# Kernel tuning notes

Measured on AMD Instinct MI355X. Metric: run time of the kernel, lower is better.

The kernel has to match this reference:

```python
import jax, jax.numpy as jnp
import numpy as np

B, S, CIN, WIDTH, COUT = 8, 256, 3, 64, 1
MODES, BW = 32, 3


def _dct_matrix(n):
    # orthonormal DCT-II matrix; inverse = transpose (DCT-III)
    k = np.arange(n)[:, None].astype(np.float64)
    x = np.arange(n)[None, :].astype(np.float64)
    m = np.sqrt(2.0 / n) * np.cos(np.pi * (x + 0.5) * k / n)
    m[0] *= 1.0 / np.sqrt(2.0)
    return jnp.asarray(m, dtype=jnp.float32)

DCT = _dct_matrix(S)  # [S, S]


def T_fwd(u):  # u: [B, C, H, W] -> spectral coefficients
    u = jnp.einsum('kh,bchw->bckw', DCT, u)
    return jnp.einsum('lw,bckw->bckl', DCT, u)


def T_inv(c):  # inverse transform (orthonormal => transpose)
    c = jnp.einsum('kh,bckw->bchw', DCT, c)
    return jnp.einsum('lw,bclw->bclh', DCT, c).transpose(0, 1, 3, 2)


def T_inv2(c):
    # straightforward version: apply M^T along both spatial dims
    c = jnp.einsum('kh,bckl->bchl', DCT, c)
    return jnp.einsum('lw,bchl->bchw', DCT, c)


def gelu(x):
    return jax.nn.gelu(x, approximate=False)


def pseudo_spectra(u, w, cout):
    # u: [B, Cin, S, S]; w: [Cin*BW*BW, cout, MODES*MODES]
    b = T_fwd(u)
    p = MODES + BW - 1
    bp = b[:, :, :p, :p]  # pad_slices (triL=0)
    # im2col matching torch.nn.Unfold channel-major ordering (c, ki, kj)
    patches = jnp.stack([bp[:, :, i:i + MODES, j:j + MODES]
                         for i in range(BW) for j in range(BW)], axis=2)
    bs, cin = u.shape[0], u.shape[1]
    xp = patches.reshape(bs, cin * BW * BW, MODES * MODES)
    om = jnp.einsum('bix,iox->box', xp, w).reshape(bs, cout, MODES, MODES)
    out = jnp.zeros((bs, cout, S, S), u.dtype).at[:, :, :MODES, :MODES].set(om)
    return T_inv2(out)


def conv1x1(x, w, b):
    return jnp.einsum('oi,bihw->bohw', w, x) + b[None, :, None, None]


def setup_inputs() -> dict:
    key = jax.random.key(0)
    ks = jax.random.split(key, 20)
    mm = MODES * MODES
    inp = {'x': jax.random.normal(ks[0], (B, S, S, CIN), dtype=jnp.float32)}
    # PseudoSpectra weights: scale * U[0,1), scale = 1/(in*out)
    inp['wl'] = jax.random.uniform(ks[1], (CIN * BW * BW, WIDTH - CIN, mm), dtype=jnp.float32) / (CIN * (WIDTH - CIN))
    for i in range(4):
        inp[f'wc{i}'] = jax.random.uniform(ks[2 + i], (WIDTH * BW * BW, WIDTH, mm), dtype=jnp.float32) / (WIDTH * WIDTH)
    for i in range(4):
        inp[f'pw{i}'] = jax.random.normal(ks[6 + i], (WIDTH, WIDTH), dtype=jnp.float32) * 0.05
        inp[f'pb{i}'] = jnp.zeros((WIDTH,), dtype=jnp.float32)
    inp['fc1_w'] = jax.random.normal(ks[10], (WIDTH, 128), dtype=jnp.float32) * 0.05
    inp['fc1_b'] = jnp.zeros((128,), dtype=jnp.float32)
    inp['fc2_w'] = jax.random.normal(ks[11], (128, COUT), dtype=jnp.float32) * 0.05
    inp['fc2_b'] = jnp.zeros((COUT,), dtype=jnp.float32)
    return inp


def reference(x, wl, wc0, wc1, wc2, wc3,
              pw0, pb0, pw1, pb1, pw2, pb2, pw3, pb3,
              fc1_w, fc1_b, fc2_w, fc2_b):
    h = x.transpose(0, 3, 1, 2)  # [B, CIN, S, S]
    h = jnp.concatenate([h, gelu(pseudo_spectra(h, wl, WIDTH - CIN))], axis=1)
    h = h + gelu(conv1x1(h, pw0, pb0) + pseudo_spectra(h, wc0, WIDTH))
    h = h + gelu(conv1x1(h, pw1, pb1) + pseudo_spectra(h, wc1, WIDTH))
    h = h + gelu(conv1x1(h, pw2, pb2) + pseudo_spectra(h, wc2, WIDTH))
    h = h + gelu(conv1x1(h, pw3, pb3) + pseudo_spectra(h, wc3, WIDTH))
    h = h.transpose(0, 2, 3, 1)  # [B, S, S, WIDTH]
    h = gelu(h @ fc1_w + fc1_b)
    h = h @ fc2_w + fc2_b  # [B, S, S, COUT]
    y = h.transpose(0, 3, 1, 2)
    y = T_fwd(T_inv2(y))  # T(T.inv(.)) along spatial dims, as in source
    return y.transpose(0, 2, 3, 1)
```

## Files before the change

kernel.cpp:

```cpp
#include <hip/hip_runtime.h>
#include <math.h>

#define BB 8
#define S 256
#define CIN 3
#define W64 64
#define MODES 32
#define PP 34
#define KPAD 36
#define KPB 40

typedef __attribute__((ext_vector_type(8))) short bfrag;
typedef __attribute__((ext_vector_type(16))) float f32x16;

__device__ __forceinline__ float gelu_f(float x){
    float z = fabsf(x) * 0.70710678118654752f;
    float t = 1.0f / (1.0f + 0.3275911f * z);
    float p = ((((1.061405429f * t - 1.453152027f) * t) + 1.421413741f) * t
               - 0.284496736f) * t + 0.254829592f;
    float e = __expf(-z * z);
    float erf = 1.0f - p * t * e;
    erf = copysignf(erf, x);
    return 0.5f * x * (1.0f + erf);
}

__device__ __forceinline__ void split_bf(float x, short &hi, short &lo){
    unsigned u = __float_as_uint(x);
    unsigned r = u + 0x7FFFu + ((u >> 16) & 1u);
    hi = (short)(r >> 16);
    float hf = __uint_as_float(r & 0xFFFF0000u);
    float l = x - hf;
    unsigned v = __float_as_uint(l);
    unsigned s2 = v + 0x7FFFu + ((v >> 16) & 1u);
    lo = (short)(s2 >> 16);
}

__device__ __forceinline__ void split8(float4 a, float4 b, bfrag &hv, bfrag &lv){
    short hi, lo;
    split_bf(a.x, hi, lo); hv[0] = hi; lv[0] = lo;
    split_bf(a.y, hi, lo); hv[1] = hi; lv[1] = lo;
    split_bf(a.z, hi, lo); hv[2] = hi; lv[2] = lo;
    split_bf(a.w, hi, lo); hv[3] = hi; lv[3] = lo;
    split_bf(b.x, hi, lo); hv[4] = hi; lv[4] = lo;
    split_bf(b.y, hi, lo); hv[5] = hi; lv[5] = lo;
    split_bf(b.z, hi, lo); hv[6] = hi; lv[6] = lo;
    split_bf(b.w, hi, lo); hv[7] = hi; lv[7] = lo;
}

__global__ void k_init_dt(float* __restrict__ dt, short* __restrict__ dth,
                          short* __restrict__ dtl){
    int tid = blockIdx.x * 256 + threadIdx.x;
    if (tid >= S * KPB) return;
    int h = tid / KPB, k = tid % KPB;
    double v = 0.0;
    if (k < PP) {
        v = sqrt(2.0 / (double)S) * cos(3.14159265358979323846 * (h + 0.5) * k / (double)S);
        if (k == 0) v *= 0.70710678118654752440;
    }
    float f = (float)v;
    if (k < KPAD) dt[h * KPAD + k] = f;
    short hi, lo; split_bf(f, hi, lo);
    dth[tid] = hi; dtl[tid] = lo;
}

__global__ void k_prep_pw(const float* __restrict__ pw, short* __restrict__ pwh,
                          short* __restrict__ pwl){
    int e = blockIdx.x * 256 + threadIdx.x;
    if (e >= 4096) return;
    short hi, lo; split_bf(pw[e], hi, lo);
    pwh[e] = hi; pwl[e] = lo;
}

__global__ void k_prep_fc1(const float* __restrict__ fc1w, short* __restrict__ f1h,
                           short* __restrict__ f1l){
    int e = blockIdx.x * 256 + threadIdx.x;
    if (e >= 8192) return;
    int i = e >> 7, j = e & 127;
    int n = j >> 5, ks = i >> 4;
    int l = (j & 31) + (((i & 15) >= 8) ? 32 : 0);
    int jr = i & 7;
    int idx = ((n * 4 + ks) * 64 + l) * 8 + jr;
    short hi, lo; split_bf(fc1w[e], hi, lo);
    f1h[idx] = hi; f1l[idx] = lo;
}

__global__ void k_copy_x(const float* __restrict__ x, float* __restrict__ h){
    int e = blockIdx.x * 256 + threadIdx.x;
    if (e >= BB * S * S * CIN) return;
    int px = e / CIN, c = e % CIN;
    h[(size_t)px * W64 + c] = x[e];
}

template<int C>
__global__ void k_fwd1(const float* __restrict__ src, float* __restrict__ tmp1,
                       const float* __restrict__ dt){
    int b = blockIdx.y;
    int idx = blockIdx.x * 256 + threadIdx.x;
    if (idx >= S * C) return;
    float acc[PP];
    #pragma unroll
    for (int k = 0; k < PP; k++) acc[k] = 0.f;
    const float* sp = src + (size_t)b * S * S * C + idx;
    for (int hh = 0; hh < S; hh++){
        float v = sp[(size_t)hh * S * C];
        const float* dr = dt + hh * KPAD;
        #pragma unroll
        for (int k = 0; k < PP; k++) acc[k] = fmaf(dr[k], v, acc[k]);
    }
    float* op = tmp1 + (size_t)b * PP * S * C + idx;
    #pragma unroll
    for (int k = 0; k < PP; k++) op[(size_t)k * S * C] = acc[k];
}

__global__ void k_fwd2_3(const float* __restrict__ tmp1, float* __restrict__ bp,
                         const float* __restrict__ dt){
    const int C = 3;
    int b = blockIdx.y;
    int idx = blockIdx.x * 256 + threadIdx.x;
    if (idx >= PP * C) return;
    int k = idx / C, c = idx % C;
    float acc[PP];
    #pragma unroll
    for (int l = 0; l < PP; l++) acc[l] = 0.f;
    const float* sp = tmp1 + ((size_t)b * PP + k) * S * C + c;
    for (int w = 0; w < S; w++){
        float v = sp[(size_t)w * C];
        const float* dr = dt + w * KPAD;
        #pragma unroll
        for (int l = 0; l < PP; l++) acc[l] = fmaf(dr[l], v, acc[l]);
    }
    float* op = bp + ((size_t)b * PP + k) * PP * C + c;
    #pragma unroll
    for (int l = 0; l < PP; l++) op[(size_t)l * C] = acc[l];
}

__global__ __launch_bounds__(256, 4) void k_fwd2_64(
        const float* __restrict__ tmp1, float* __restrict__ bp,
        const float* __restrict__ dt){
    const int C = 64;
    __shared__ float red[4 * PP * 66];
    int k = blockIdx.x, b = blockIdx.y;
    int t = threadIdx.x;
    int c = t & 63;
    int ws = __builtin_amdgcn_readfirstlane(t >> 6);
    float acc[PP];
    #pragma unroll
    for (int l = 0; l < PP; l++) acc[l] = 0.f;
    const float* sp = tmp1 + ((size_t)b * PP + k) * S * C + c;
    for (int w = ws * 64; w < ws * 64 + 64; w++){
        float v = sp[(size_t)w * C];
        const float* dr = dt + w * KPAD;
        #pragma unroll
        for (int l = 0; l < PP; l++) acc[l] = fmaf(dr[l], v, acc[l]);
    }
    #pragma unroll
    for (int l = 0; l < PP; l++) red[(ws * PP + l) * 66 + c] = acc[l];
    __syncthreads();
    float* op = bp + ((size_t)b * PP + k) * PP * C;
    for (int e = t; e < PP * C; e += 256){
        int l = e >> 6, cc = e & 63;
        op[e] = red[(0 * PP + l) * 66 + cc] + red[(1 * PP + l) * 66 + cc]
              + red[(2 * PP + l) * 66 + cc] + red[(3 * PP + l) * 66 + cc];
    }
}

template<int C, int CC>
__global__ void k_xp_gather(const float* __restrict__ bp, float* __restrict__ xp){
    __shared__ float lds[8 * 3 * PP * (CC + 1)];
    int k  = blockIdx.x;
    int c0 = blockIdx.y * CC;
    int t  = threadIdx.x;
    const int TOT = 8 * 3 * PP * CC;
    for (int e = t; e < TOT; e += 256){
        int b   = e / (3 * PP * CC);
        int r   = e % (3 * PP * CC);
        int row = r / (PP * CC);
        int r2  = r % (PP * CC);
        int l   = r2 / CC;
        int c   = r2 % CC;
        lds[((b * 3 + row) * PP + l) * (CC + 1) + c] =
            bp[(((size_t)b * PP + (k + row)) * PP + l) * C + c0 + c];
    }
    __syncthreads();
    int l = t >> 3;
    int b = t & 7;
    for (int c = 0; c < CC; c++){
        #pragma unroll
        for (int ij = 0; ij < 9; ij++){
            int i_ = ij / 3, j_ = ij % 3;
            int i  = (c0 + c) * 9 + ij;
            float v = lds[((b * 3 + i_) * PP + (l + j_)) * (CC + 1) + c];
            xp[((size_t)i * 1024 + k * 32 + l) * 8 + b] = v;
        }
    }
}

template<int ITOT, int O>
__global__ void k_om(const float* __restrict__ xp, const float* __restrict__ w,
                     float* __restrict__ part){
    int bx  = blockIdx.x;
    int klt = bx & 31;
    int ot  = (bx >> 5) & 7;
    int ns  = bx >> 8;
    const int ILEN = ITOT / 3;
    int t  = threadIdx.x;
    int kl = klt * 32 + (t & 31);
    int o  = ot * 8 + (t >> 5);
    if (o >= O) return;
    float a0=0,a1=0,a2=0,a3=0,a4=0,a5=0,a6=0,a7=0;
    const float* xpp = xp + ((size_t)(ns * ILEN) * 1024 + kl) * 8;
    const float* wp  = w + ((size_t)(ns * ILEN) * O + o) * 1024 + kl;
    #pragma unroll 4
    for (int i = 0; i < ILEN; i++){
        float4 xa = *(const float4*)(xpp + (size_t)i * 8192);
        float4 xb = *(const float4*)(xpp + (size_t)i * 8192 + 4);
        float wv  = wp[(size_t)i * O * 1024];
        a0 = fmaf(xa.x, wv, a0); a1 = fmaf(xa.y, wv, a1);
        a2 = fmaf(xa.z, wv, a2); a3 = fmaf(xa.w, wv, a3);
        a4 = fmaf(xb.x, wv, a4); a5 = fmaf(xb.y, wv, a5);
        a6 = fmaf(xb.z, wv, a6); a7 = fmaf(xb.w, wv, a7);
    }
    float* pp = part + (size_t)ns * 8 * 64 * 1024;
    pp[((size_t)0 * 64 + o) * 1024 + kl] = a0;
    pp[((size_t)1 * 64 + o) * 1024 + kl] = a1;
    pp[((size_t)2 * 64 + o) * 1024 + kl] = a2;
    pp[((size_t)3 * 64 + o) * 1024 + kl] = a3;
    pp[((size_t)4 * 64 + o) * 1024 + kl] = a4;
    pp[((size_t)5 * 64 + o) * 1024 + kl] = a5;
    pp[((size_t)6 * 64 + o) * 1024 + kl] = a6;
    pp[((size_t)7 * 64 + o) * 1024 + kl] = a7;
}

template<int O>
__global__ void k_inv1(const float* __restrict__ part, float* __restrict__ t2,
                       const float* __restrict__ dt){
    __shared__ float oms[32 * 65];
    const int N = 8 * 64 * 1024;
    int wc = blockIdx.x, k = blockIdx.y, b = blockIdx.z;
    int t = threadIdx.x;
    for (int e = t; e < 2048; e += 256){
        int o_ = e >> 5, l = e & 31;
        int idx = ((b * 64 + o_) << 10) + k * 32 + l;
        oms[l * 65 + o_] = part[idx] + part[N + idx] + part[2 * N + idx];
    }
    __syncthreads();
    int o  = t & 63;
    int wg = __builtin_amdgcn_readfirstlane(t >> 6);
    int wbase = wc * 32 + wg * 8;
    float acc[8];
    #pragma unroll
    for (int wj = 0; wj < 8; wj++) acc[wj] = 0.f;
    for (int l = 0; l < 32; l++){
        float ov = oms[l * 65 + o];
        #pragma unroll
        for (int wj = 0; wj < 8; wj++)
            acc[wj] = fmaf(dt[(wbase + wj) * KPAD + l], ov, acc[wj]);
    }
    if (o < O){
        #pragma unroll
        for (int wj = 0; wj < 8; wj++)
            t2[(((size_t)b * 32 + k) * S + wbase + wj) * 64 + o] = acc[wj];
    }
}

template<bool CONV>
__global__ __launch_bounds__(256, 5) void k_fused(
        const float* __restrict__ t2, float* __restrict__ h,
        const short* __restrict__ pwh, const short* __restrict__ pwl,
        const float* __restrict__ pb,
        const short* __restrict__ dth, const short* __restrict__ dtl){
    __shared__ short t2fh[8 * 64 * 8];
    __shared__ short t2fl[8 * 64 * 8];
    __shared__ short hsfh[CONV ? 8 * 64 * 8 : 1];
    __shared__ short hsfl[CONV ? 8 * 64 * 8 : 1];
    int wt = blockIdx.x, b = blockIdx.y;
    int t = threadIdx.x;

    #pragma unroll
    for (int e2 = 0; e2 < 2; e2++){
        int e = t + e2 * 256;
        int le = e & 63, ks = (e >> 6) & 1, ne = e >> 7;
        int oe = (ne & 1) * 32 + (le & 31);
        int we = wt * 2 + (ne >> 1);
        int k0 = ks * 16 + (le >> 5) * 8;
        bfrag hv, lv;
        #pragma unroll
        for (int j = 0; j < 8; j++){
            short hi, lo;
            split_bf(t2[((size_t)(b * 32 + k0 + j) * S + we) * 64 + oe], hi, lo);
            hv[j] = hi; lv[j] = lo;
        }
        int idx = ((ne * 2 + ks) * 64 + le) * 8;
        *(bfrag*)(t2fh + idx) = hv;
        *(bfrag*)(t2fl + idx) = lv;
    }

    int l = t & 63;
    int n = t >> 6;
    int oh = n & 1, wl = n >> 1;
    int o = oh * 32 + (l & 31);

    int ihalf = t & 7;
    int pxA = t >> 3;
    int pxB = pxA + 32;
    const float* hb = h + ((size_t)b * S * S + (size_t)wt * 2) * 64;
    size_t offA = ((size_t)(pxA >> 1) * S + (pxA & 1)) * 64 + ihalf * 8;
    size_t offB = ((size_t)(pxB >> 1) * S + (pxB & 1)) * 64 + ihalf * 8;
    float4 a0, a1, b0, b1;
    if (CONV){
        a0 = *(const float4*)(hb + offA);
        a1 = *(const float4*)(hb + offA + 4);
        b0 = *(const float4*)(hb + offB);
        b1 = *(const float4*)(hb + offB + 4);
    }

    for (int ht = 0; ht < 8; ht++){
        if (CONV){
            int ks = ihalf >> 1;
            int lh = (ihalf & 1) * 32;
            int g  = (pxA & 1) * 4 + ks;
            bfrag hv, lv;
            split8(a0, a1, hv, lv);
            int rowA = (pxA >> 1) + lh;
            *(bfrag*)(hsfh + (g * 64 + (rowA ^ g)) * 8) = hv;
            *(bfrag*)(hsfl + (g * 64 + (rowA ^ g)) * 8) = lv;
            split8(b0, b1, hv, lv);
            int rowB = (pxB >> 1) + lh;
            *(bfrag*)(hsfh + (g * 64 + (rowB ^ g)) * 8) = hv;
            *(bfrag*)(hsfl + (g * 64 + (rowB ^ g)) * 8) = lv;
        }
        __syncthreads();
        if (CONV && ht < 7){
            const float* hb2 = hb + (size_t)(ht + 1) * 32 * S * 64;
            a0 = *(const float4*)(hb2 + offA);
            a1 = *(const float4*)(hb2 + offA + 4);
            b0 = *(const float4*)(hb2 + offB);
            b1 = *(const float4*)(hb2 + offB + 4);
        }

        f32x16 acc = {0,0,0,0,0,0,0,0,0,0,0,0,0,0,0,0};

        int hh0 = ht * 32;
        #pragma unroll
        for (int ks = 0; ks < 2; ks++){
            int aoff = (hh0 + (l & 31)) * KPB + ks * 16 + (l >> 5) * 8;
            bfrag ah = *(const bfrag*)(dth + aoff);
            bfrag al = *(const bfrag*)(dtl + aoff);
            int boff = ((n * 2 + ks) * 64 + l) * 8;
            bfrag bh = *(const bfrag*)(t2fh + boff);
            bfrag bl = *(const bfrag*)(t2fl + boff);
            acc = __builtin_amdgcn_mfma_f32_32x32x16_bf16(ah, bh, acc, 0, 0, 0);
            acc = __builtin_amdgcn_mfma_f32_32x32x16_bf16(ah, bl, acc, 0, 0, 0);
            acc = __builtin_amdgcn_mfma_f32_32x32x16_bf16(al, bh, acc, 0, 0, 0);
        }

        if (CONV){
            #pragma unroll
            for (int ks = 0; ks < 4; ks++){
                int g = wl * 4 + ks;
                int aoff = (g * 64 + (l ^ g)) * 8;
                bfrag ah = *(const bfrag*)(hsfh + aoff);
                bfrag al = *(const bfrag*)(hsfl + aoff);
                int boff = o * 64 + ks * 16 + (l >> 5) * 8;
                bfrag bh = *(const bfrag*)(pwh + boff);
                bfrag bl = *(const bfrag*)(pwl + boff);
                acc = __builtin_amdgcn_mfma_f32_32x32x16_bf16(ah, bh, acc, 0, 0, 0);
                acc = __builtin_amdgcn_mfma_f32_32x32x16_bf16(ah, bl, acc, 0, 0, 0);
                acc = __builtin_amdgcn_mfma_f32_32x32x16_bf16(al, bh, acc, 0, 0, 0);
            }
            float pbv = pb[o];
            #pragma unroll
            for (int r = 0; r < 16; r++){
                int row = (r & 3) + 8 * (r >> 2) + 4 * (l >> 5);
                size_t pix = ((size_t)b * S + ht * 32 + row) * S + wt * 2 + wl;
                float res = h[pix * 64 + o];
                h[pix * 64 + o] = res + gelu_f(acc[r] + pbv);
            }
        } else {
            if (o < 61){
                #pragma unroll
                for (int r = 0; r < 16; r++){
                    int row = (r & 3) + 8 * (r >> 2) + 4 * (l >> 5);
                    size_t pix = ((size_t)b * S + ht * 32 + row) * S + wt * 2 + wl;
                    h[pix * 64 + 3 + o] = gelu_f(acc[r]);
                }
            }
        }
        __syncthreads();
    }
}

__global__ __launch_bounds__(256, 4) void k_mlp(
        const float* __restrict__ h, const short* __restrict__ f1h,
        const short* __restrict__ f1l, const float* __restrict__ fc1b,
        const float* __restrict__ fc2w, const float* __restrict__ fc2b,
        float* __restrict__ out){
    __shared__ short ah_[2 * 4 * 64 * 8];
    __shared__ short al_[2 * 4 * 64 * 8];
    __shared__ float red[2 * 64 * 33];
    size_t base = (size_t)blockIdx.x * 64;
    int t = threadIdx.x;
    const float* hrow = h + base * 64;
    #pragma unroll
    for (int e2 = 0; e2 < 2; e2++){
        int e = t + e2 * 256;
        int px = e >> 3, ih = e & 7;
        float4 v0 = *(const float4*)(hrow + px * 64 + ih * 8);
        float4 v1 = *(const float4*)(hrow + px * 64 + ih * 8 + 4);
        bfrag hv, lv;
        split8(v0, v1, hv, lv);
        int g = (px >> 5) * 4 + (ih >> 1);
        int row = (px & 31) + (ih & 1) * 32;
        *(bfrag*)(ah_ + (g * 64 + (row ^ g)) * 8) = hv;
        *(bfrag*)(al_ + (g * 64 + (row ^ g)) * 8) = lv;
    }
    __syncthreads();
    int l = t & 63;
    int w = t >> 6;
    int m = w >> 1;
    int n0 = (w & 1) * 2;
    f32x16 acc0 = {0,0,0,0,0,0,0,0,0,0,0,0,0,0,0,0};
    f32x16 acc1 = {0,0,0,0,0,0,0,0,0,0,0,0,0,0,0,0};
    #pragma unroll
    for (int ks = 0; ks < 4; ks++){
        int g = m * 4 + ks;
        int aoff = (g * 64 + (l ^ g)) * 8;
        bfrag ah = *(const bfrag*)(ah_ + aoff);
        bfrag al = *(const bfrag*)(al_ + aoff);
        int b0off = ((n0 * 4 + ks) * 64 + l) * 8;
        int b1off = (((n0 + 1) * 4 + ks) * 64 + l) * 8;
        bfrag b0h = *(const bfrag*)(f1h + b0off);
        bfrag b0l = *(const bfrag*)(f1l + b0off);
        bfrag b1h = *(const bfrag*)(f1h + b1off);
        bfrag b1l = *(const bfrag*)(f1l + b1off);
        acc0 = __builtin_amdgcn_mfma_f32_32x32x16_bf16(ah, b0h, acc0, 0, 0, 0);
        acc0 = __builtin_amdgcn_mfma_f32_32x32x16_bf16(ah, b0l, acc0, 0, 0, 0);
        acc0 = __builtin_amdgcn_mfma_f32_32x32x16_bf16(al, b0h, acc0, 0, 0, 0);
        acc1 = __builtin_amdgcn_mfma_f32_32x32x16_bf16(ah, b1h, acc1, 0, 0, 0);
        acc1 = __builtin_amdgcn_mfma_f32_32x32x16_bf16(ah, b1l, acc1, 0, 0, 0);
        acc1 = __builtin_amdgcn_mfma_f32_32x32x16_bf16(al, b1h, acc1, 0, 0, 0);
    }
    int j0 = n0 * 32 + (l & 31), j1 = j0 + 32;
    float b10 = fc1b[j0], b11 = fc1b[j1];
    float f20 = fc2w[j0], f21 = fc2w[j1];
    float* rb = red + (w & 1) * 64 * 33;
    #pragma unroll
    for (int r = 0; r < 16; r++){
        int row = (r & 3) + 8 * (r >> 2) + 4 * (l >> 5);
        rb[(m * 32 + row) * 33 + (l & 31)] =
            gelu_f(acc0[r] + b10) * f20 + gelu_f(acc1[r] + b11) * f21;
    }
    __syncthreads();
    if (t < 64){
        float s = fc2b[0];
        #pragma unroll
        for (int c = 0; c < 32; c++)
            s += red[t * 33 + c] + red[(64 + t) * 33 + c];
        out[base + t] = s;
    }
}

extern "C" void kernel_launch(void* const* d_in, const int* in_sizes, int n_in,
                              void* d_out, int out_size, void* d_ws, size_t ws_size,
                              hipStream_t stream) {
    const float* x    = (const float*)d_in[0];
    const float* wl   = (const float*)d_in[1];
    const float* wc[4] = {(const float*)d_in[2], (const float*)d_in[3],
                          (const float*)d_in[4], (const float*)d_in[5]};
    const float* pw[4] = {(const float*)d_in[6], (const float*)d_in[8],
                          (const float*)d_in[10], (const float*)d_in[12]};
    const float* pb[4] = {(const float*)d_in[7], (const float*)d_in[9],
                          (const float*)d_in[11], (const float*)d_in[13]};
    const float* fc1w = (const float*)d_in[14];
    const float* fc1b = (const float*)d_in[15];
    const float* fc2w = (const float*)d_in[16];
    const float* fc2b = (const float*)d_in[17];
    float* out = (float*)d_out;

    char* ws = (char*)d_ws;
    size_t off = 0;
    float* dt   = (float*)(ws + off); off += (size_t)S * KPAD * 4;
    short* dth  = (short*)(ws + off); off += (size_t)S * KPB * 2;
    short* dtl  = (short*)(ws + off); off += (size_t)S * KPB * 2;
    short* pwh  = (short*)(ws + off); off += (size_t)4 * 4096 * 2;
    short* pwl  = (short*)(ws + off); off += (size_t)4 * 4096 * 2;
    short* f1h  = (short*)(ws + off); off += (size_t)8192 * 2;
    short* f1l  = (short*)(ws + off); off += (size_t)8192 * 2;
    float* h    = (float*)(ws + off); off += (size_t)BB * S * S * W64 * 4;
    float* tmp1 = (float*)(ws + off); off += (size_t)BB * PP * S * W64 * 4;
    float* bp   = (float*)(ws + off); off += (size_t)BB * PP * PP * W64 * 4;
    float* xp   = (float*)(ws + off); off += (size_t)576 * 1024 * 8 * 4;
    float* part = (float*)(ws + off); off += (size_t)3 * 8 * 64 * 1024 * 4;
    float* t2   = (float*)(ws + off); off += (size_t)BB * 32 * S * W64 * 4;

    k_init_dt<<<(S * KPB + 255) / 256, 256, 0, stream>>>(dt, dth, dtl);
    for (int i = 0; i < 4; i++)
        k_prep_pw<<<16, 256, 0, stream>>>(pw[i], pwh + i * 4096, pwl + i * 4096);
    k_prep_fc1<<<32, 256, 0, stream>>>(fc1w, f1h, f1l);
    k_copy_x<<<(BB * S * S * CIN + 255) / 256, 256, 0, stream>>>(x, h);

    k_fwd1<3><<<dim3(3, BB), 256, 0, stream>>>(x, tmp1, dt);
    k_fwd2_3<<<dim3(1, BB), 256, 0, stream>>>(tmp1, bp, dt);
    k_xp_gather<3, 3><<<dim3(32, 1), 256, 0, stream>>>(bp, xp);
    k_om<27, 61><<<768, 256, 0, stream>>>(xp, wl, part);
    k_inv1<61><<<dim3(8, 32, BB), 256, 0, stream>>>(part, t2, dt);
    k_fused<false><<<dim3(128, BB), 256, 0, stream>>>(
        t2, h, nullptr, nullptr, nullptr, dth, dtl);

    for (int blk = 0; blk < 4; blk++){
        k_fwd1<64><<<dim3(64, BB), 256, 0, stream>>>(h, tmp1, dt);
        k_fwd2_64<<<dim3(PP, BB), 256, 0, stream>>>(tmp1, bp, dt);
        k_xp_gather<64, 16><<<dim3(32, 4), 256, 0, stream>>>(bp, xp);
        k_om<576, 64><<<768, 256, 0, stream>>>(xp, wc[blk], part);
        k_inv1<64><<<dim3(8, 32, BB), 256, 0, stream>>>(part, t2, dt);
        k_fused<true><<<dim3(128, BB), 256, 0, stream>>>(
            t2, h, pwh + blk * 4096, pwl + blk * 4096, pb[blk], dth, dtl);
    }

    k_mlp<<<dim3(BB * S * S / 64), 256, 0, stream>>>(h, f1h, f1l, fc1b, fc2w, fc2b, out);
}
```

Baseline: 1.322 ms.

## Split forward DCT over H halves and double-buffer LDS in fused kernel

The first forward-transform pass for the 64-channel blocks now splits the H reduction into two halves, one per block. This doubles the grid, and the two partial results are summed when the second pass reads them. In the fused conv/inverse kernel, the bf16-split input tile is double-buffered in LDS, which drops one barrier per row tile. The residual is now rebuilt from the hi+lo LDS copy instead of being reloaded from global memory. This costs extra workspace, an extra read in the second pass, slightly lower residual precision, and a lower occupancy hint.

```diff
diff --git a/kernel.cpp b/kernel.cpp
--- a/kernel.cpp
+++ b/kernel.cpp
@@ -45,6 +45,10 @@
     split_bf(b.y, hi, lo); hv[5] = hi; lv[5] = lo;
     split_bf(b.z, hi, lo); hv[6] = hi; lv[6] = lo;
     split_bf(b.w, hi, lo); hv[7] = hi; lv[7] = lo;
+}
+
+__device__ __forceinline__ float bf2f(short s){
+    return __uint_as_float(((unsigned)(unsigned short)s) << 16);
 }
 
 __global__ void k_init_dt(float* __restrict__ dt, short* __restrict__ dth,
@@ -112,6 +116,27 @@
     for (int k = 0; k < PP; k++) op[(size_t)k * S * C] = acc[k];
 }
 
+__global__ void k_fwd1_64s(const float* __restrict__ src, float* __restrict__ tmp1,
+                           const float* __restrict__ dt){
+    const int C = 64;
+    const size_t TM1 = (size_t)BB * PP * S * C;
+    int b = blockIdx.z, hf = blockIdx.y;
+    int idx = blockIdx.x * 256 + threadIdx.x;
+    float acc[PP];
+    #pragma unroll
+    for (int k = 0; k < PP; k++) acc[k] = 0.f;
+    const float* sp = src + (size_t)b * S * S * C + (size_t)hf * 128 * S * C + idx;
+    for (int hh = 0; hh < 128; hh++){
+        float v = sp[(size_t)hh * S * C];
+        const float* dr = dt + (hf * 128 + hh) * KPAD;
+        #pragma unroll
+        for (int k = 0; k < PP; k++) acc[k] = fmaf(dr[k], v, acc[k]);
+    }
+    float* op = tmp1 + (size_t)hf * TM1 + (size_t)b * PP * S * C + idx;
+    #pragma unroll
+    for (int k = 0; k < PP; k++) op[(size_t)k * S * C] = acc[k];
+}
+
 __global__ void k_fwd2_3(const float* __restrict__ tmp1, float* __restrict__ bp,
                          const float* __restrict__ dt){
     const int C = 3;
@@ -138,6 +163,7 @@
         const float* __restrict__ tmp1, float* __restrict__ bp,
         const float* __restrict__ dt){
     const int C = 64;
+    const size_t TM1 = (size_t)BB * PP * S * C;
     __shared__ float red[4 * PP * 66];
     int k = blockIdx.x, b = blockIdx.y;
     int t = threadIdx.x;
@@ -148,7 +174,7 @@
     for (int l = 0; l < PP; l++) acc[l] = 0.f;
     const float* sp = tmp1 + ((size_t)b * PP + k) * S * C + c;
     for (int w = ws * 64; w < ws * 64 + 64; w++){
-        float v = sp[(size_t)w * C];
+        float v = sp[(size_t)w * C] + sp[TM1 + (size_t)w * C];
         const float* dr = dt + w * KPAD;
         #pragma unroll
         for (int l = 0; l < PP; l++) acc[l] = fmaf(dr[l], v, acc[l]);
@@ -264,15 +290,15 @@
 }
 
 template<bool CONV>
-__global__ __launch_bounds__(256, 5) void k_fused(
+__global__ __launch_bounds__(256, 3) void k_fused(
         const float* __restrict__ t2, float* __restrict__ h,
         const short* __restrict__ pwh, const short* __restrict__ pwl,
         const float* __restrict__ pb,
         const short* __restrict__ dth, const short* __restrict__ dtl){
     __shared__ short t2fh[8 * 64 * 8];
     __shared__ short t2fl[8 * 64 * 8];
-    __shared__ short hsfh[CONV ? 8 * 64 * 8 : 1];
-    __shared__ short hsfl[CONV ? 8 * 64 * 8 : 1];
+    __shared__ short hsfh[CONV ? 2 * 8 * 64 * 8 : 1];
+    __shared__ short hsfl[CONV ? 2 * 8 * 64 * 8 : 1];
     int wt = blockIdx.x, b = blockIdx.y;
     int t = threadIdx.x;
 
@@ -299,6 +325,10 @@
     int n = t >> 6;
     int oh = n & 1, wl = n >> 1;
     int o = oh * 32 + (l & 31);
+
+    int g_res = wl * 4 + (o >> 4);
+    int jres  = o & 7;
+    int rowadd = ((o & 15) >= 8) ? 32 : 0;
 
     int ihalf = t & 7;
     int pxA = t >> 3;
@@ -314,6 +344,7 @@
         b1 = *(const float4*)(hb + offB + 4);
     }
 
+    int cur = 0;
     for (int ht = 0; ht < 8; ht++){
         if (CONV){
             int ks = ihalf >> 1;
@@ -322,14 +353,16 @@
             bfrag hv, lv;
             split8(a0, a1, hv, lv);
             int rowA = (pxA >> 1) + lh;
-            *(bfrag*)(hsfh + (g * 64 + (rowA ^ g)) * 8) = hv;
-            *(bfrag*)(hsfl + (g * 64 + (rowA ^ g)) * 8) = lv;
+            *(bfrag*)(hsfh + cur * 4096 + (g * 64 + (rowA ^ g)) * 8) = hv;
+            *(bfrag*)(hsfl + cur * 4096 + (g * 64 + (rowA ^ g)) * 8) = lv;
             split8(b0, b1, hv, lv);
             int rowB = (pxB >> 1) + lh;
-            *(bfrag*)(hsfh + (g * 64 + (rowB ^ g)) * 8) = hv;
-            *(bfrag*)(hsfl + (g * 64 + (rowB ^ g)) * 8) = lv;
+            *(bfrag*)(hsfh + cur * 4096 + (g * 64 + (rowB ^ g)) * 8) = hv;
+            *(bfrag*)(hsfl + cur * 4096 + (g * 64 + (rowB ^ g)) * 8) = lv;
+            __syncthreads();
+        } else {
+            if (ht == 0) __syncthreads();
         }
-        __syncthreads();
         if (CONV && ht < 7){
             const float* hb2 = hb + (size_t)(ht + 1) * 32 * S * 64;
             a0 = *(const float4*)(hb2 + offA);
@@ -358,7 +391,7 @@
             #pragma unroll
             for (int ks = 0; ks < 4; ks++){
                 int g = wl * 4 + ks;
-                int aoff = (g * 64 + (l ^ g)) * 8;
+                int aoff = cur * 4096 + (g * 64 + (l ^ g)) * 8;
                 bfrag ah = *(const bfrag*)(hsfh + aoff);
                 bfrag al = *(const bfrag*)(hsfl + aoff);
                 int boff = o * 64 + ks * 16 + (l >> 5) * 8;
@@ -372,10 +405,12 @@
             #pragma unroll
             for (int r = 0; r < 16; r++){
                 int row = (r & 3) + 8 * (r >> 2) + 4 * (l >> 5);
+                int ei = cur * 4096 + (g_res * 64 + ((row + rowadd) ^ g_res)) * 8 + jres;
+                float res = bf2f(hsfh[ei]) + bf2f(hsfl[ei]);
                 size_t pix = ((size_t)b * S + ht * 32 + row) * S + wt * 2 + wl;
-                float res = h[pix * 64 + o];
                 h[pix * 64 + o] = res + gelu_f(acc[r] + pbv);
             }
+            cur ^= 1;
         } else {
             if (o < 61){
                 #pragma unroll
@@ -386,7 +421,6 @@
                 }
             }
         }
-        __syncthreads();
     }
 }
 
@@ -487,7 +521,7 @@
     short* f1h  = (short*)(ws + off); off += (size_t)8192 * 2;
     short* f1l  = (short*)(ws + off); off += (size_t)8192 * 2;
     float* h    = (float*)(ws + off); off += (size_t)BB * S * S * W64 * 4;
-    float* tmp1 = (float*)(ws + off); off += (size_t)BB * PP * S * W64 * 4;
+    float* tmp1 = (float*)(ws + off); off += (size_t)2 * BB * PP * S * W64 * 4;
     float* bp   = (float*)(ws + off); off += (size_t)BB * PP * PP * W64 * 4;
     float* xp   = (float*)(ws + off); off += (size_t)576 * 1024 * 8 * 4;
     float* part = (float*)(ws + off); off += (size_t)3 * 8 * 64 * 1024 * 4;
@@ -508,7 +542,7 @@
         t2, h, nullptr, nullptr, nullptr, dth, dtl);
 
     for (int blk = 0; blk < 4; blk++){
-        k_fwd1<64><<<dim3(64, BB), 256, 0, stream>>>(h, tmp1, dt);
+        k_fwd1_64s<<<dim3(64, 2, BB), 256, 0, stream>>>(h, tmp1, dt);
         k_fwd2_64<<<dim3(PP, BB), 256, 0, stream>>>(tmp1, bp, dt);
         k_xp_gather<64, 16><<<dim3(32, 4), 256, 0, stream>>>(bp, xp);
         k_om<576, 64><<<768, 256, 0, stream>>>(xp, wc[blk], part);
```

After: 1.172 ms. -11.4%, faster.
